# Kernel tuning notes

Hardware: AMD Instinct MI355X
Metric: run time of the kernel (lower is better)

## Reference

```python
import jax, jax.numpy as jnp
import numpy as np

V, D, C, NUM_CLASSES = 50000, 128, 128, 200
N, S = 4096, 128
NUM_VIDEOS = 256
KSIZES = (3, 4, 5)


def setup_inputs() -> dict:
    key = jax.random.key(0)
    ks = jax.random.split(key, 10)
    input_x = jax.random.randint(ks[0], (N, 1, S), 0, V)
    # sorted segment ids, every video non-empty (contiguous ragged segments)
    segment_ids = ((jnp.arange(N) * NUM_VIDEOS) // N).astype(jnp.int32)
    emb = jax.random.normal(ks[1], (V, D), dtype=jnp.float32) * (2.0 / (V + D)) ** 0.5  # xavier_normal
    W3 = jax.random.normal(ks[2], (3, D, C), dtype=jnp.float32) * 0.05
    b3 = jnp.zeros((C,), dtype=jnp.float32)
    W4 = jax.random.normal(ks[3], (4, D, C), dtype=jnp.float32) * 0.05
    b4 = jnp.zeros((C,), dtype=jnp.float32)
    W5 = jax.random.normal(ks[4], (5, D, C), dtype=jnp.float32) * 0.05
    b5 = jnp.zeros((C,), dtype=jnp.float32)
    Wout = jax.random.normal(ks[5], (3 * C, NUM_CLASSES), dtype=jnp.float32) * 0.05
    bout = jnp.zeros((NUM_CLASSES,), dtype=jnp.float32)
    return {"input_x": input_x, "segment_ids": segment_ids, "emb": emb,
            "W3": W3, "b3": b3, "W4": W4, "b4": b4, "W5": W5, "b5": b5,
            "Wout": Wout, "bout": bout}


def _conv_maxpool(x, W, b):
    # x: [N, S, D], W: [w, D, C] -> conv over time (VALID), then max over time -> [N, C]
    y = jax.lax.conv_general_dilated(x, W, window_strides=(1,), padding='VALID',
                                     dimension_numbers=('NWC', 'WIO', 'NWC')) + b
    return jnp.max(y, axis=1)


def reference(input_x, segment_ids, emb, W3, b3, W4, b4, W5, b5, Wout, bout):
    x = emb[input_x[:, 0, :]]                       # [N, S, D]
    feat = jnp.concatenate([_conv_maxpool(x, W3, b3),
                            _conv_maxpool(x, W4, b4),
                            _conv_maxpool(x, W5, b5)], axis=1)  # [N, 3C]
    logits = feat @ Wout + bout                     # [N, num_classes]
    scores = jax.nn.sigmoid(logits)
    # ragged per-video max over contiguous text rows
    video_scores = jax.ops.segment_max(scores, segment_ids, num_segments=NUM_VIDEOS)
    return video_scores
```

## Files before the change

kernel.cpp:

```cpp
#include <hip/hip_runtime.h>
#include <hip/hip_bf16.h>


using bf16_t  = __bf16;
using bf16x4  = __attribute__((ext_vector_type(4))) __bf16;
using bf16x8  = __attribute__((ext_vector_type(8))) __bf16;
using floatx4 = __attribute__((ext_vector_type(4))) float;

#define N_SENT 4096
#define S_LEN  128
#define D_DIM  128
#define C_DIM  128
#define NCLS   200
#define NVID   256
#define V_SZ   50000

#define X_ROWS   132
#define X_STRIDE 136

#define BP3_OFF 0
#define BP4_OFF 49152
#define BP5_OFF 114688
#define BPACK_ELEMS 196608

#define FEAT_OFF  (1u << 20)
#define EMB16_OFF (8u << 20)

__global__ void prep_emb(const float* __restrict__ emb, bf16_t* __restrict__ emb16) {
  int i4 = blockIdx.x * 256 + threadIdx.x;
  const floatx4 f = __builtin_nontemporal_load((const floatx4*)emb + i4);
  bf16x4 h;
  h.x = (bf16_t)f.x; h.y = (bf16_t)f.y; h.z = (bf16_t)f.z; h.w = (bf16_t)f.w;
  __builtin_nontemporal_store(h, (bf16x4*)emb16 + i4);
}

__global__ void prep_bpack(const float* __restrict__ W3,
                           const float* __restrict__ W4,
                           const float* __restrict__ W5,
                           bf16_t* __restrict__ bpack) {
  int idx = blockIdx.x * 256 + threadIdx.x;
  if (idx >= BPACK_ELEMS) return;
  int KS; const float* W; int rel;
  if (idx < BP4_OFF)      { KS = 3; W = W3; rel = idx; }
  else if (idx < BP5_OFF) { KS = 4; W = W4; rel = idx - BP4_OFF; }
  else                    { KS = 5; W = W5; rel = idx - BP5_OFF; }
  int szct  = 2048 * KS;
  int ctile = rel / szct;
  int r2    = rel - ctile * szct;
  int g     = r2 >> 7;
  int r3    = r2 & 127;
  int n     = r3 >> 3;
  int j     = r3 & 7;
  bpack[idx] = (bf16_t)W[(g * 8 + j) * C_DIM + (ctile * 16 + n)];
}

template <int KS>
__device__ __forceinline__ void conv_k(const bf16_t* Xs_lane,
                                       const bf16_t* bp0, const bf16_t* bp1,
                                       const float* __restrict__ bk,
                                       float* __restrict__ feat,
                                       int m, int q, int lane, int sent,
                                       int koff, int ct0) {
  floatx4 acc[2][8];
#pragma unroll
  for (int ct = 0; ct < 2; ++ct)
#pragma unroll
    for (int mt = 0; mt < 8; ++mt)
      acc[ct][mt] = (floatx4){0.f, 0.f, 0.f, 0.f};

  const bf16_t* Arow = Xs_lane;

#pragma unroll 1
  for (int c0 = 0; c0 < KS; ++c0) {
    bf16x8 bfr0[4], bfr1[4];
#pragma unroll
    for (int st = 0; st < 4; ++st) {
      bfr0[st] = *(const bf16x8*)(bp0 + st * 512);
      bfr1[st] = *(const bf16x8*)(bp1 + st * 512);
    }
    bp0 += 2048;
    bp1 += 2048;
#pragma unroll
    for (int mt = 0; mt < 8; ++mt) {
#pragma unroll
      for (int st = 0; st < 4; ++st) {
        const bf16x8 a = *(const bf16x8*)(Arow + mt * 16 * X_STRIDE + st * 32);
        acc[0][mt] = __builtin_amdgcn_mfma_f32_16x16x32_bf16(a, bfr0[st], acc[0][mt], 0, 0, 0);
        acc[1][mt] = __builtin_amdgcn_mfma_f32_16x16x32_bf16(a, bfr1[st], acc[1][mt], 0, 0, 0);
      }
    }
    Arow += X_STRIDE;
  }

  const int tlim = S_LEN - KS + 1;
#pragma unroll
  for (int ct = 0; ct < 2; ++ct) {
    float mx = -__builtin_inff();
#pragma unroll
    for (int mt = 0; mt < 8; ++mt)
#pragma unroll
      for (int r = 0; r < 4; ++r) {
        const int t = mt * 16 + q * 4 + r;
        if (t < tlim) mx = fmaxf(mx, acc[ct][mt][r]);
      }
    mx = fmaxf(mx, __shfl_xor(mx, 16));
    mx = fmaxf(mx, __shfl_xor(mx, 32));
    const int c = (ct0 + ct) * 16 + m;
    if (lane < 16)
      __builtin_nontemporal_store(mx + bk[c], &feat[sent * 384 + koff + c]);
  }
}

__global__ __launch_bounds__(256, 3) void conv_gemm(
    const int* __restrict__ input_x, const bf16_t* __restrict__ emb16,
    const bf16_t* __restrict__ bpack, const float* __restrict__ b3,
    const float* __restrict__ b4, const float* __restrict__ b5,
    float* __restrict__ feat) {
  __shared__ __align__(16) bf16_t Xs[X_ROWS * X_STRIDE];
  const int sent = blockIdx.x;
  const int tid  = threadIdx.x;

  {
    const int rip = tid >> 4;
    const int l16 = tid & 15;
#pragma unroll
    for (int r0 = 0; r0 < S_LEN; r0 += 16) {
      const int row   = r0 + rip;
      const int token = __builtin_nontemporal_load(&input_x[sent * S_LEN + row]);
      const bf16x8 v  =
          __builtin_nontemporal_load((const bf16x8*)(emb16 + token * D_DIM + l16 * 8));
      *(bf16x8*)(&Xs[row * X_STRIDE + l16 * 8]) = v;
    }
    for (int i = tid; i < 4 * X_STRIDE; i += 256)
      Xs[128 * X_STRIDE + i] = (bf16_t)0.f;
  }
  __syncthreads();

  const int wv   = tid >> 6;
  const int lane = tid & 63;
  const int m    = lane & 15;
  const int q    = lane >> 4;
  const bf16_t* Xs_lane = Xs + m * X_STRIDE + q * 8;
  const int     ct0     = 2 * wv;
  const int     blaneoff = q * 128 + m * 8;

  conv_k<3>(Xs_lane, bpack + BP3_OFF + (ct0 + 0) * (2048 * 3) + blaneoff,
            bpack + BP3_OFF + (ct0 + 1) * (2048 * 3) + blaneoff,
            b3, feat, m, q, lane, sent, 0, ct0);
  __builtin_amdgcn_sched_barrier(0);
  conv_k<4>(Xs_lane, bpack + BP4_OFF + (ct0 + 0) * (2048 * 4) + blaneoff,
            bpack + BP4_OFF + (ct0 + 1) * (2048 * 4) + blaneoff,
            b4, feat, m, q, lane, sent, 128, ct0);
  __builtin_amdgcn_sched_barrier(0);
  conv_k<5>(Xs_lane, bpack + BP5_OFF + (ct0 + 0) * (2048 * 5) + blaneoff,
            bpack + BP5_OFF + (ct0 + 1) * (2048 * 5) + blaneoff,
            b5, feat, m, q, lane, sent, 256, ct0);
}

__global__ void classify(const float* __restrict__ feat,
                         const float* __restrict__ Wout,
                         const float* __restrict__ bout,
                         float* __restrict__ out) {
  __shared__ float fs[16 * 384];
  const int vid = blockIdx.x;
  const int tid = threadIdx.x;
  for (int i = tid; i < 16 * 384; i += 256) fs[i] = feat[vid * 16 * 384 + i];
  __syncthreads();
  if (tid < NCLS) {
    float acc[16];
#pragma unroll
    for (int s = 0; s < 16; ++s) acc[s] = 0.f;
    for (int d = 0; d < 384; ++d) {
      const float wv = Wout[d * NCLS + tid];
#pragma unroll
      for (int s = 0; s < 16; ++s) acc[s] = fmaf(fs[s * 384 + d], wv, acc[s]);
    }
    const float b = bout[tid];
    float vmax = -__builtin_inff();
#pragma unroll
    for (int s = 0; s < 16; ++s) {
      const float sc = 1.f / (1.f + __expf(-(acc[s] + b)));
      vmax = fmaxf(vmax, sc);
    }
    out[vid * NCLS + tid] = vmax;
  }
}

extern "C" void kernel_launch(void* const* d_in, const int* in_sizes, int n_in,
                              void* d_out, int out_size, void* d_ws, size_t ws_size,
                              hipStream_t stream) {
  const int*   input_x = (const int*)d_in[0];
  const float* emb  = (const float*)d_in[2];
  const float* W3   = (const float*)d_in[3];
  const float* b3   = (const float*)d_in[4];
  const float* W4   = (const float*)d_in[5];
  const float* b4   = (const float*)d_in[6];
  const float* W5   = (const float*)d_in[7];
  const float* b5   = (const float*)d_in[8];
  const float* Wout = (const float*)d_in[9];
  const float* bout = (const float*)d_in[10];

  bf16_t* bpack = (bf16_t*)d_ws;
  float*  feat  = (float*)((char*)d_ws + FEAT_OFF);
  bf16_t* emb16 = (bf16_t*)((char*)d_ws + EMB16_OFF);
  float*  out   = (float*)d_out;

  prep_emb<<<(V_SZ * D_DIM) / 4 / 256, 256, 0, stream>>>(emb, emb16);
  prep_bpack<<<BPACK_ELEMS / 256, 256, 0, stream>>>(W3, W4, W5, bpack);
  conv_gemm<<<N_SENT, 256, 0, stream>>>(input_x, emb16, bpack, b3, b4, b5, feat);
  classify<<<NVID, 256, 0, stream>>>(feat, Wout, bout, out);
}
```

Before: 293.6 us.

## Switch conv GEMM to 32x32x16 MFMA with two sentences per block

The conv kernel now uses 32x32x16 bf16 MFMA instead of 16x16x32, with weights repacked to match. Each block processes two sentences, and each wave covers one sentence and 64 channels, prefetching the next B fragment. The larger tiles reduce LDS A-fragment reads per FLOP. The classifier inner loop is also vectorised to read four features at once from shared memory. The trade-offs are fewer blocks, lower occupancy (launch bounds 2), larger accumulators and higher register pressure.

```diff
diff --git a/kernel.cpp b/kernel.cpp
--- a/kernel.cpp
+++ b/kernel.cpp
@@ -2,10 +2,11 @@
 #include <hip/hip_bf16.h>
 
 
-using bf16_t  = __bf16;
-using bf16x4  = __attribute__((ext_vector_type(4))) __bf16;
-using bf16x8  = __attribute__((ext_vector_type(8))) __bf16;
-using floatx4 = __attribute__((ext_vector_type(4))) float;
+using bf16_t   = __bf16;
+using bf16x4   = __attribute__((ext_vector_type(4))) __bf16;
+using bf16x8   = __attribute__((ext_vector_type(8))) __bf16;
+using floatx4  = __attribute__((ext_vector_type(4))) float;
+using floatx16 = __attribute__((ext_vector_type(16))) float;
 
 #define N_SENT 4096
 #define S_LEN  128
@@ -44,124 +45,127 @@
   if (idx < BP4_OFF)      { KS = 3; W = W3; rel = idx; }
   else if (idx < BP5_OFF) { KS = 4; W = W4; rel = idx - BP4_OFF; }
   else                    { KS = 5; W = W5; rel = idx - BP5_OFF; }
-  int szct  = 2048 * KS;
-  int ctile = rel / szct;
-  int r2    = rel - ctile * szct;
-  int g     = r2 >> 7;
-  int r3    = r2 & 127;
-  int n     = r3 >> 3;
-  int j     = r3 & 7;
-  bpack[idx] = (bf16_t)W[(g * 8 + j) * C_DIM + (ctile * 16 + n)];
+  const int per_ct = 4096 * KS;
+  const int ctile  = rel / per_ct;
+  const int r2     = rel - ctile * per_ct;
+  const int t      = r2 >> 9;
+  const int r3     = r2 & 511;
+  const int lane   = r3 >> 3;
+  const int j      = r3 & 7;
+  const int n  = lane & 31;
+  const int h  = lane >> 5;
+  const int c0 = t >> 3;
+  const int kk = t & 7;
+  const int d  = kk * 16 + h * 8 + j;
+  const int c  = ctile * 32 + n;
+  bpack[idx] = (bf16_t)W[(c0 * D_DIM + d) * C_DIM + c];
 }
 
 template <int KS>
-__device__ __forceinline__ void conv_k(const bf16_t* Xs_lane,
-                                       const bf16_t* bp0, const bf16_t* bp1,
-                                       const float* __restrict__ bk,
-                                       float* __restrict__ feat,
-                                       int m, int q, int lane, int sent,
-                                       int koff, int ct0) {
-  floatx4 acc[2][8];
-#pragma unroll
-  for (int ct = 0; ct < 2; ++ct)
-#pragma unroll
-    for (int mt = 0; mt < 8; ++mt)
-      acc[ct][mt] = (floatx4){0.f, 0.f, 0.f, 0.f};
-
-  const bf16_t* Arow = Xs_lane;
-
-#pragma unroll 1
-  for (int c0 = 0; c0 < KS; ++c0) {
-    bf16x8 bfr0[4], bfr1[4];
-#pragma unroll
-    for (int st = 0; st < 4; ++st) {
-      bfr0[st] = *(const bf16x8*)(bp0 + st * 512);
-      bfr1[st] = *(const bf16x8*)(bp1 + st * 512);
-    }
-    bp0 += 2048;
-    bp1 += 2048;
-#pragma unroll
-    for (int mt = 0; mt < 8; ++mt) {
-#pragma unroll
-      for (int st = 0; st < 4; ++st) {
-        const bf16x8 a = *(const bf16x8*)(Arow + mt * 16 * X_STRIDE + st * 32);
-        acc[0][mt] = __builtin_amdgcn_mfma_f32_16x16x32_bf16(a, bfr0[st], acc[0][mt], 0, 0, 0);
-        acc[1][mt] = __builtin_amdgcn_mfma_f32_16x16x32_bf16(a, bfr1[st], acc[1][mt], 0, 0, 0);
-      }
-    }
-    Arow += X_STRIDE;
+__device__ __forceinline__ void conv_k32(const bf16_t* __restrict__ Ab,
+                                         const bf16_t* bp0, const bf16_t* bp1,
+                                         const float* __restrict__ bk,
+                                         float* __restrict__ feat,
+                                         int sent, int koff, int cbase, int lane) {
+  floatx16 acc[2][4] = {};
+
+  const int NT = 8 * KS;
+  bf16x8 bc0 = *(const bf16x8*)bp0;  bp0 += 512;
+  bf16x8 bc1 = *(const bf16x8*)bp1;  bp1 += 512;
+
+#pragma unroll 2
+  for (int t = 0; t < NT; ++t) {
+    const bf16x8 bn0 = *(const bf16x8*)bp0;
+    const bf16x8 bn1 = *(const bf16x8*)bp1;
+    bp0 += 512; bp1 += 512;
+
+    const bf16_t* Ar = Ab + (t >> 3) * X_STRIDE + (t & 7) * 16;
+#pragma unroll
+    for (int mt = 0; mt < 4; ++mt) {
+      const bf16x8 a = *(const bf16x8*)(Ar + mt * 32 * X_STRIDE);
+      acc[0][mt] = __builtin_amdgcn_mfma_f32_32x32x16_bf16(a, bc0, acc[0][mt], 0, 0, 0);
+      acc[1][mt] = __builtin_amdgcn_mfma_f32_32x32x16_bf16(a, bc1, acc[1][mt], 0, 0, 0);
+    }
+    bc0 = bn0; bc1 = bn1;
   }
 
   const int tlim = S_LEN - KS + 1;
+  const int h = lane >> 5;
+  const int n = lane & 31;
 #pragma unroll
   for (int ct = 0; ct < 2; ++ct) {
     float mx = -__builtin_inff();
 #pragma unroll
-    for (int mt = 0; mt < 8; ++mt)
-#pragma unroll
-      for (int r = 0; r < 4; ++r) {
-        const int t = mt * 16 + q * 4 + r;
-        if (t < tlim) mx = fmaxf(mx, acc[ct][mt][r]);
+    for (int mt = 0; mt < 4; ++mt)
+#pragma unroll
+      for (int r = 0; r < 16; ++r) {
+        const int tt = mt * 32 + (r & 3) + 8 * (r >> 2) + 4 * h;
+        if (tt < tlim) mx = fmaxf(mx, acc[ct][mt][r]);
       }
-    mx = fmaxf(mx, __shfl_xor(mx, 16));
     mx = fmaxf(mx, __shfl_xor(mx, 32));
-    const int c = (ct0 + ct) * 16 + m;
-    if (lane < 16)
+    const int c = cbase + ct * 32 + n;
+    if (lane < 32)
       __builtin_nontemporal_store(mx + bk[c], &feat[sent * 384 + koff + c]);
   }
 }
 
-__global__ __launch_bounds__(256, 3) void conv_gemm(
+__global__ __launch_bounds__(256, 2) void conv_gemm(
     const int* __restrict__ input_x, const bf16_t* __restrict__ emb16,
     const bf16_t* __restrict__ bpack, const float* __restrict__ b3,
     const float* __restrict__ b4, const float* __restrict__ b5,
     float* __restrict__ feat) {
-  __shared__ __align__(16) bf16_t Xs[X_ROWS * X_STRIDE];
-  const int sent = blockIdx.x;
-  const int tid  = threadIdx.x;
+  __shared__ __align__(16) bf16_t Xs[2 * X_ROWS * X_STRIDE];
+  const int sent0 = blockIdx.x * 2;
+  const int tid   = threadIdx.x;
 
   {
     const int rip = tid >> 4;
     const int l16 = tid & 15;
 #pragma unroll
-    for (int r0 = 0; r0 < S_LEN; r0 += 16) {
-      const int row   = r0 + rip;
-      const int token = __builtin_nontemporal_load(&input_x[sent * S_LEN + row]);
+    for (int r0 = 0; r0 < 2 * S_LEN; r0 += 16) {
+      const int row = r0 + rip;
+      const int s   = row >> 7;
+      const int r   = row & 127;
+      const int token = __builtin_nontemporal_load(&input_x[(sent0 + s) * S_LEN + r]);
       const bf16x8 v  =
           __builtin_nontemporal_load((const bf16x8*)(emb16 + token * D_DIM + l16 * 8));
-      *(bf16x8*)(&Xs[row * X_STRIDE + l16 * 8]) = v;
-    }
-    for (int i = tid; i < 4 * X_STRIDE; i += 256)
-      Xs[128 * X_STRIDE + i] = (bf16_t)0.f;
+      *(bf16x8*)(&Xs[(s * X_ROWS + r) * X_STRIDE + l16 * 8]) = v;
+    }
+    for (int i = tid; i < 2 * 4 * X_STRIDE; i += 256) {
+      const int s = (i >= 4 * X_STRIDE);
+      const int o = i - s * (4 * X_STRIDE);
+      Xs[(s * X_ROWS + 128) * X_STRIDE + o] = (bf16_t)0.f;
+    }
   }
   __syncthreads();
 
-  const int wv   = tid >> 6;
-  const int lane = tid & 63;
-  const int m    = lane & 15;
-  const int q    = lane >> 4;
-  const bf16_t* Xs_lane = Xs + m * X_STRIDE + q * 8;
-  const int     ct0     = 2 * wv;
-  const int     blaneoff = q * 128 + m * 8;
-
-  conv_k<3>(Xs_lane, bpack + BP3_OFF + (ct0 + 0) * (2048 * 3) + blaneoff,
-            bpack + BP3_OFF + (ct0 + 1) * (2048 * 3) + blaneoff,
-            b3, feat, m, q, lane, sent, 0, ct0);
+  const int wv    = tid >> 6;
+  const int lane  = tid & 63;
+  const int s     = wv >> 1;
+  const int cpair = wv & 1;
+  const bf16_t* Ab = Xs + (s * X_ROWS + (lane & 31)) * X_STRIDE + (lane >> 5) * 8;
+  const int sent  = sent0 + s;
+  const int cbase = cpair * 64;
+  const int blo   = lane * 8;
+
+  conv_k32<3>(Ab, bpack + BP3_OFF + (cpair * 2 + 0) * (4096 * 3) + blo,
+                  bpack + BP3_OFF + (cpair * 2 + 1) * (4096 * 3) + blo,
+              b3, feat, sent, 0, cbase, lane);
   __builtin_amdgcn_sched_barrier(0);
-  conv_k<4>(Xs_lane, bpack + BP4_OFF + (ct0 + 0) * (2048 * 4) + blaneoff,
-            bpack + BP4_OFF + (ct0 + 1) * (2048 * 4) + blaneoff,
-            b4, feat, m, q, lane, sent, 128, ct0);
+  conv_k32<4>(Ab, bpack + BP4_OFF + (cpair * 2 + 0) * (4096 * 4) + blo,
+                  bpack + BP4_OFF + (cpair * 2 + 1) * (4096 * 4) + blo,
+              b4, feat, sent, 128, cbase, lane);
   __builtin_amdgcn_sched_barrier(0);
-  conv_k<5>(Xs_lane, bpack + BP5_OFF + (ct0 + 0) * (2048 * 5) + blaneoff,
-            bpack + BP5_OFF + (ct0 + 1) * (2048 * 5) + blaneoff,
-            b5, feat, m, q, lane, sent, 256, ct0);
+  conv_k32<5>(Ab, bpack + BP5_OFF + (cpair * 2 + 0) * (4096 * 5) + blo,
+                  bpack + BP5_OFF + (cpair * 2 + 1) * (4096 * 5) + blo,
+              b5, feat, sent, 256, cbase, lane);
 }
 
 __global__ void classify(const float* __restrict__ feat,
                          const float* __restrict__ Wout,
                          const float* __restrict__ bout,
                          float* __restrict__ out) {
-  __shared__ float fs[16 * 384];
+  __shared__ __align__(16) float fs[16 * 384];
   const int vid = blockIdx.x;
   const int tid = threadIdx.x;
   for (int i = tid; i < 16 * 384; i += 256) fs[i] = feat[vid * 16 * 384 + i];
@@ -170,10 +174,19 @@
     float acc[16];
 #pragma unroll
     for (int s = 0; s < 16; ++s) acc[s] = 0.f;
-    for (int d = 0; d < 384; ++d) {
-      const float wv = Wout[d * NCLS + tid];
-#pragma unroll
-      for (int s = 0; s < 16; ++s) acc[s] = fmaf(fs[s * 384 + d], wv, acc[s]);
+    for (int d = 0; d < 384; d += 4) {
+      const float w0 = Wout[(d + 0) * NCLS + tid];
+      const float w1 = Wout[(d + 1) * NCLS + tid];
+      const float w2 = Wout[(d + 2) * NCLS + tid];
+      const float w3 = Wout[(d + 3) * NCLS + tid];
+#pragma unroll
+      for (int s = 0; s < 16; ++s) {
+        const floatx4 f = *(const floatx4*)&fs[s * 384 + d];
+        acc[s] = fmaf(f.x, w0, acc[s]);
+        acc[s] = fmaf(f.y, w1, acc[s]);
+        acc[s] = fmaf(f.z, w2, acc[s]);
+        acc[s] = fmaf(f.w, w3, acc[s]);
+      }
     }
     const float b = bout[tid];
     float vmax = -__builtin_inff();
@@ -207,6 +220,6 @@
 
   prep_emb<<<(V_SZ * D_DIM) / 4 / 256, 256, 0, stream>>>(emb, emb16);
   prep_bpack<<<BPACK_ELEMS / 256, 256, 0, stream>>>(W3, W4, W5, bpack);
-  conv_gemm<<<N_SENT, 256, 0, stream>>>(input_x, emb16, bpack, b3, b4, b5, feat);
+  conv_gemm<<<N_SENT / 2, 256, 0, stream>>>(input_x, emb16, bpack, b3, b4, b5, feat);
   classify<<<NVID, 256, 0, stream>>>(feat, Wout, bout, out);
 }
```

Result: slower. 319.9 us (+9.0%).

## Split conv GEMM waves 2x2 over time rows and channels with LDS max reduction

Applied to the files above, without the earlier changes.

Changes the per-wave tiling in conv_gemm from all 128 time rows by 2 channel tiles to 64 time rows by 4 channel tiles. Each wave now loads half as many A fragments from LDS per B fragment and reuses each A fragment across four MFMAs. Each wave still does the same number of MFMAs, but it holds twice as many B fragments in registers. Partial maxima from the two time halves are combined through a small shared array and a barrier before the bias is added and feat is stored. This adds register pressure and an extra sync.

```diff
diff --git a/kernel.cpp b/kernel.cpp
--- a/kernel.cpp
+++ b/kernel.cpp
@@ -55,59 +55,57 @@
 }
 
 template <int KS>
-__device__ __forceinline__ void conv_k(const bf16_t* Xs_lane,
+__device__ __forceinline__ void conv_k(const bf16_t* Ab,
                                        const bf16_t* bp0, const bf16_t* bp1,
-                                       const float* __restrict__ bk,
-                                       float* __restrict__ feat,
-                                       int m, int q, int lane, int sent,
-                                       int koff, int ct0) {
-  floatx4 acc[2][8];
-#pragma unroll
-  for (int ct = 0; ct < 2; ++ct)
-#pragma unroll
-    for (int mt = 0; mt < 8; ++mt)
+                                       const bf16_t* bp2, const bf16_t* bp3,
+                                       float* __restrict__ pms,
+                                       int m, int q, int lane, int rbase) {
+  floatx4 acc[4][4];
+#pragma unroll
+  for (int ct = 0; ct < 4; ++ct)
+#pragma unroll
+    for (int mt = 0; mt < 4; ++mt)
       acc[ct][mt] = (floatx4){0.f, 0.f, 0.f, 0.f};
-
-  const bf16_t* Arow = Xs_lane;
 
 #pragma unroll 1
   for (int c0 = 0; c0 < KS; ++c0) {
-    bf16x8 bfr0[4], bfr1[4];
+    bf16x8 B0[4], B1[4], B2[4], B3[4];
 #pragma unroll
     for (int st = 0; st < 4; ++st) {
-      bfr0[st] = *(const bf16x8*)(bp0 + st * 512);
-      bfr1[st] = *(const bf16x8*)(bp1 + st * 512);
-    }
-    bp0 += 2048;
-    bp1 += 2048;
-#pragma unroll
-    for (int mt = 0; mt < 8; ++mt) {
+      B0[st] = *(const bf16x8*)(bp0 + st * 512);
+      B1[st] = *(const bf16x8*)(bp1 + st * 512);
+      B2[st] = *(const bf16x8*)(bp2 + st * 512);
+      B3[st] = *(const bf16x8*)(bp3 + st * 512);
+    }
+    bp0 += 2048; bp1 += 2048; bp2 += 2048; bp3 += 2048;
+#pragma unroll
+    for (int mt = 0; mt < 4; ++mt) {
 #pragma unroll
       for (int st = 0; st < 4; ++st) {
-        const bf16x8 a = *(const bf16x8*)(Arow + mt * 16 * X_STRIDE + st * 32);
-        acc[0][mt] = __builtin_amdgcn_mfma_f32_16x16x32_bf16(a, bfr0[st], acc[0][mt], 0, 0, 0);
-        acc[1][mt] = __builtin_amdgcn_mfma_f32_16x16x32_bf16(a, bfr1[st], acc[1][mt], 0, 0, 0);
+        const bf16x8 a = *(const bf16x8*)(Ab + mt * 16 * X_STRIDE + st * 32);
+        acc[0][mt] = __builtin_amdgcn_mfma_f32_16x16x32_bf16(a, B0[st], acc[0][mt], 0, 0, 0);
+        acc[1][mt] = __builtin_amdgcn_mfma_f32_16x16x32_bf16(a, B1[st], acc[1][mt], 0, 0, 0);
+        acc[2][mt] = __builtin_amdgcn_mfma_f32_16x16x32_bf16(a, B2[st], acc[2][mt], 0, 0, 0);
+        acc[3][mt] = __builtin_amdgcn_mfma_f32_16x16x32_bf16(a, B3[st], acc[3][mt], 0, 0, 0);
       }
     }
-    Arow += X_STRIDE;
+    Ab += X_STRIDE;
   }
 
   const int tlim = S_LEN - KS + 1;
 #pragma unroll
-  for (int ct = 0; ct < 2; ++ct) {
+  for (int ct = 0; ct < 4; ++ct) {
     float mx = -__builtin_inff();
 #pragma unroll
-    for (int mt = 0; mt < 8; ++mt)
+    for (int mt = 0; mt < 4; ++mt)
 #pragma unroll
       for (int r = 0; r < 4; ++r) {
-        const int t = mt * 16 + q * 4 + r;
+        const int t = rbase + mt * 16 + q * 4 + r;
         if (t < tlim) mx = fmaxf(mx, acc[ct][mt][r]);
       }
     mx = fmaxf(mx, __shfl_xor(mx, 16));
     mx = fmaxf(mx, __shfl_xor(mx, 32));
-    const int c = (ct0 + ct) * 16 + m;
-    if (lane < 16)
-      __builtin_nontemporal_store(mx + bk[c], &feat[sent * 384 + koff + c]);
+    if (lane < 16) pms[ct * 16 + m] = mx;
   }
 }
 
@@ -117,6 +115,7 @@
     const float* __restrict__ b4, const float* __restrict__ b5,
     float* __restrict__ feat) {
   __shared__ __align__(16) bf16_t Xs[X_ROWS * X_STRIDE];
+  __shared__ float pm[3 * 2 * 128];
   const int sent = blockIdx.x;
   const int tid  = threadIdx.x;
 
@@ -140,21 +139,40 @@
   const int lane = tid & 63;
   const int m    = lane & 15;
   const int q    = lane >> 4;
-  const bf16_t* Xs_lane = Xs + m * X_STRIDE + q * 8;
-  const int     ct0     = 2 * wv;
-  const int     blaneoff = q * 128 + m * 8;
-
-  conv_k<3>(Xs_lane, bpack + BP3_OFF + (ct0 + 0) * (2048 * 3) + blaneoff,
-            bpack + BP3_OFF + (ct0 + 1) * (2048 * 3) + blaneoff,
-            b3, feat, m, q, lane, sent, 0, ct0);
+  const int mh   = wv >> 1;
+  const int ch   = wv & 1;
+  const bf16_t* Ab = Xs + (mh * 64 + m) * X_STRIDE + q * 8;
+  const int blaneoff = q * 128 + m * 8;
+  const int cb   = ch * 4;
+
+  conv_k<3>(Ab, bpack + BP3_OFF + (cb + 0) * 6144 + blaneoff,
+                bpack + BP3_OFF + (cb + 1) * 6144 + blaneoff,
+                bpack + BP3_OFF + (cb + 2) * 6144 + blaneoff,
+                bpack + BP3_OFF + (cb + 3) * 6144 + blaneoff,
+            &pm[(0 * 2 + mh) * 128 + ch * 64], m, q, lane, mh * 64);
   __builtin_amdgcn_sched_barrier(0);
-  conv_k<4>(Xs_lane, bpack + BP4_OFF + (ct0 + 0) * (2048 * 4) + blaneoff,
-            bpack + BP4_OFF + (ct0 + 1) * (2048 * 4) + blaneoff,
-            b4, feat, m, q, lane, sent, 128, ct0);
+  conv_k<4>(Ab, bpack + BP4_OFF + (cb + 0) * 8192 + blaneoff,
+                bpack + BP4_OFF + (cb + 1) * 8192 + blaneoff,
+                bpack + BP4_OFF + (cb + 2) * 8192 + blaneoff,
+                bpack + BP4_OFF + (cb + 3) * 8192 + blaneoff,
+            &pm[(1 * 2 + mh) * 128 + ch * 64], m, q, lane, mh * 64);
   __builtin_amdgcn_sched_barrier(0);
-  conv_k<5>(Xs_lane, bpack + BP5_OFF + (ct0 + 0) * (2048 * 5) + blaneoff,
-            bpack + BP5_OFF + (ct0 + 1) * (2048 * 5) + blaneoff,
-            b5, feat, m, q, lane, sent, 256, ct0);
+  conv_k<5>(Ab, bpack + BP5_OFF + (cb + 0) * 10240 + blaneoff,
+                bpack + BP5_OFF + (cb + 1) * 10240 + blaneoff,
+                bpack + BP5_OFF + (cb + 2) * 10240 + blaneoff,
+                bpack + BP5_OFF + (cb + 3) * 10240 + blaneoff,
+            &pm[(2 * 2 + mh) * 128 + ch * 64], m, q, lane, mh * 64);
+
+  __syncthreads();
+
+  for (int i = tid; i < 384; i += 256) {
+    const int sec = i >> 7;
+    const int c   = i & 127;
+    const float v = fmaxf(pm[(sec * 2 + 0) * 128 + c],
+                          pm[(sec * 2 + 1) * 128 + c]);
+    const float* bs = (sec == 0) ? b3 : ((sec == 1) ? b4 : b5);
+    __builtin_nontemporal_store(v + bs[c], &feat[sent * 384 + i]);
+  }
 }
 
 __global__ void classify(const float* __restrict__ feat,
```

New measurement: 301.5 us. +2.7%, slower.

## Fuse classifier matvec into conv kernel with atomic segment max

Applied to the files above, without the earlier changes.

Moves the output projection into the conv kernel. Each block keeps its 384 pooled features in LDS, computes its 200 logits against a transposed Wout using readlane broadcasts, and merges them into per-video maxima with atomicMax on order-preserving integer keys. A small finalize kernel adds the bias and applies the sigmoid after the max, relying on sigmoid being monotonic. This removes the feat round-trip through global memory and the separate classify kernel. In exchange it adds a transpose/zeroing prep kernel, 256-way atomic contention per video and a serial scalar dot-product tail in each conv block.

```diff
diff --git a/kernel.cpp b/kernel.cpp
--- a/kernel.cpp
+++ b/kernel.cpp
@@ -23,8 +23,14 @@
 #define BP5_OFF 114688
 #define BPACK_ELEMS 196608
 
-#define FEAT_OFF  (1u << 20)
+#define WOUTT_OFF (512u << 10)
+#define KEYS_OFF  (1u << 20)
 #define EMB16_OFF (8u << 20)
+
+__device__ __forceinline__ float rdlane(float v, int sl) {
+  return __builtin_bit_cast(float,
+      __builtin_amdgcn_readlane(__builtin_bit_cast(int, v), sl));
+}
 
 __global__ void prep_emb(const float* __restrict__ emb, bf16_t* __restrict__ emb16) {
   int i4 = blockIdx.x * 256 + threadIdx.x;
@@ -54,12 +60,24 @@
   bpack[idx] = (bf16_t)W[(g * 8 + j) * C_DIM + (ctile * 16 + n)];
 }
 
+__global__ void prep_aux(const float* __restrict__ Wout,
+                         float* __restrict__ woutT,
+                         unsigned* __restrict__ keys) {
+  const int b = blockIdx.x;
+  const int t = threadIdx.x;
+  if (b < 384) {
+    if (t < NCLS) woutT[t * 384 + b] = Wout[b * NCLS + t];
+  } else {
+    keys[(b - 384) * 256 + t] = 0u;
+  }
+}
+
 template <int KS>
 __device__ __forceinline__ void conv_k(const bf16_t* Xs_lane,
                                        const bf16_t* bp0, const bf16_t* bp1,
                                        const float* __restrict__ bk,
-                                       float* __restrict__ feat,
-                                       int m, int q, int lane, int sent,
+                                       float* __restrict__ fb,
+                                       int m, int q, int lane,
                                        int koff, int ct0) {
   floatx4 acc[2][8];
 #pragma unroll
@@ -106,8 +124,7 @@
     mx = fmaxf(mx, __shfl_xor(mx, 16));
     mx = fmaxf(mx, __shfl_xor(mx, 32));
     const int c = (ct0 + ct) * 16 + m;
-    if (lane < 16)
-      __builtin_nontemporal_store(mx + bk[c], &feat[sent * 384 + koff + c]);
+    if (lane < 16) fb[koff + c] = mx + bk[c];
   }
 }
 
@@ -115,8 +132,9 @@
     const int* __restrict__ input_x, const bf16_t* __restrict__ emb16,
     const bf16_t* __restrict__ bpack, const float* __restrict__ b3,
     const float* __restrict__ b4, const float* __restrict__ b5,
-    float* __restrict__ feat) {
+    const float* __restrict__ woutT, unsigned* __restrict__ keys) {
   __shared__ __align__(16) bf16_t Xs[X_ROWS * X_STRIDE];
+  __shared__ __align__(16) float fb[384];
   const int sent = blockIdx.x;
   const int tid  = threadIdx.x;
 
@@ -146,44 +164,53 @@
 
   conv_k<3>(Xs_lane, bpack + BP3_OFF + (ct0 + 0) * (2048 * 3) + blaneoff,
             bpack + BP3_OFF + (ct0 + 1) * (2048 * 3) + blaneoff,
-            b3, feat, m, q, lane, sent, 0, ct0);
+            b3, fb, m, q, lane, 0, ct0);
   __builtin_amdgcn_sched_barrier(0);
   conv_k<4>(Xs_lane, bpack + BP4_OFF + (ct0 + 0) * (2048 * 4) + blaneoff,
             bpack + BP4_OFF + (ct0 + 1) * (2048 * 4) + blaneoff,
-            b4, feat, m, q, lane, sent, 128, ct0);
+            b4, fb, m, q, lane, 128, ct0);
   __builtin_amdgcn_sched_barrier(0);
   conv_k<5>(Xs_lane, bpack + BP5_OFF + (ct0 + 0) * (2048 * 5) + blaneoff,
             bpack + BP5_OFF + (ct0 + 1) * (2048 * 5) + blaneoff,
-            b5, feat, m, q, lane, sent, 256, ct0);
-}
-
-__global__ void classify(const float* __restrict__ feat,
-                         const float* __restrict__ Wout,
+            b5, fb, m, q, lane, 256, ct0);
+
+  __syncthreads();
+
+  float fl[6];
+#pragma unroll
+  for (int j = 0; j < 6; ++j) fl[j] = fb[lane + 64 * j];
+
+  const int cls = (tid < NCLS) ? tid : 0;
+  const float* wrow = woutT + cls * 384;
+  float acc = 0.f;
+#pragma unroll
+  for (int jj = 0; jj < 6; ++jj) {
+#pragma unroll 4
+    for (int dd = 0; dd < 64; dd += 4) {
+      const floatx4 w = *(const floatx4*)(wrow + jj * 64 + dd);
+      acc = fmaf(w.x, rdlane(fl[jj], dd + 0), acc);
+      acc = fmaf(w.y, rdlane(fl[jj], dd + 1), acc);
+      acc = fmaf(w.z, rdlane(fl[jj], dd + 2), acc);
+      acc = fmaf(w.w, rdlane(fl[jj], dd + 3), acc);
+    }
+  }
+
+  if (tid < NCLS) {
+    const unsigned b   = __builtin_bit_cast(unsigned, acc);
+    const unsigned key = (b & 0x80000000u) ? ~b : (b | 0x80000000u);
+    atomicMax(&keys[(sent >> 4) * NCLS + tid], key);
+  }
+}
+
+__global__ void finalize(const unsigned* __restrict__ keys,
                          const float* __restrict__ bout,
                          float* __restrict__ out) {
-  __shared__ float fs[16 * 384];
-  const int vid = blockIdx.x;
-  const int tid = threadIdx.x;
-  for (int i = tid; i < 16 * 384; i += 256) fs[i] = feat[vid * 16 * 384 + i];
-  __syncthreads();
-  if (tid < NCLS) {
-    float acc[16];
-#pragma unroll
-    for (int s = 0; s < 16; ++s) acc[s] = 0.f;
-    for (int d = 0; d < 384; ++d) {
-      const float wv = Wout[d * NCLS + tid];
-#pragma unroll
-      for (int s = 0; s < 16; ++s) acc[s] = fmaf(fs[s * 384 + d], wv, acc[s]);
-    }
-    const float b = bout[tid];
-    float vmax = -__builtin_inff();
-#pragma unroll
-    for (int s = 0; s < 16; ++s) {
-      const float sc = 1.f / (1.f + __expf(-(acc[s] + b)));
-      vmax = fmaxf(vmax, sc);
-    }
-    out[vid * NCLS + tid] = vmax;
-  }
+  const int c = threadIdx.x;
+  const int i = blockIdx.x * NCLS + c;
+  const unsigned u = keys[i];
+  const unsigned b = (u & 0x80000000u) ? (u & 0x7FFFFFFFu) : ~u;
+  const float logit = __builtin_bit_cast(float, b) + bout[c];
+  out[i] = 1.f / (1.f + __expf(-logit));
 }
 
 extern "C" void kernel_launch(void* const* d_in, const int* in_sizes, int n_in,
@@ -200,13 +227,16 @@
   const float* Wout = (const float*)d_in[9];
   const float* bout = (const float*)d_in[10];
 
-  bf16_t* bpack = (bf16_t*)d_ws;
-  float*  feat  = (float*)((char*)d_ws + FEAT_OFF);
-  bf16_t* emb16 = (bf16_t*)((char*)d_ws + EMB16_OFF);
-  float*  out   = (float*)d_out;
+  bf16_t*   bpack = (bf16_t*)d_ws;
+  float*    woutT = (float*)((char*)d_ws + WOUTT_OFF);
+  unsigned* keys  = (unsigned*)((char*)d_ws + KEYS_OFF);
+  bf16_t*   emb16 = (bf16_t*)((char*)d_ws + EMB16_OFF);
+  float*    out   = (float*)d_out;
 
   prep_emb<<<(V_SZ * D_DIM) / 4 / 256, 256, 0, stream>>>(emb, emb16);
   prep_bpack<<<BPACK_ELEMS / 256, 256, 0, stream>>>(W3, W4, W5, bpack);
-  conv_gemm<<<N_SENT, 256, 0, stream>>>(input_x, emb16, bpack, b3, b4, b5, feat);
-  classify<<<NVID, 256, 0, stream>>>(feat, Wout, bout, out);
-}
+  prep_aux<<<384 + 200, 256, 0, stream>>>(Wout, woutT, keys);
+  conv_gemm<<<N_SENT, 256, 0, stream>>>(input_x, emb16, bpack, b3, b4, b5,
+                                        woutT, keys);
+  finalize<<<NVID, NCLS, 0, stream>>>(keys, bout, out);
+}
```

Measured after the change: 340.2 us. 15.9% more time.
